# Kernel tuning notes

Measured on AMD Instinct MI355X. Metric: run time of the kernel, lower is better.

Reference implementation:

```python
import jax, jax.numpy as jnp
import numpy as np

N_EMBED = 1024
N_HEADS = 16
HEAD_SIZE = N_EMBED // N_HEADS
BLOCK_SIZE = 256
LN_EPS = 1e-5


def _layernorm(x, g, b):
    mu = jnp.mean(x, axis=-1, keepdims=True)
    var = jnp.var(x, axis=-1, keepdims=True)
    return (x - mu) * jax.lax.rsqrt(var + LN_EPS) * g + b


def setup_inputs() -> dict:
    key = jax.random.key(0)
    ks = jax.random.split(key, 12)
    B, T, C, H, D = 64, 256, N_EMBED, N_HEADS, HEAD_SIZE
    s = lambda fan_in: 1.0 / np.sqrt(fan_in)
    return {
        "x": jax.random.normal(ks[0], (B, T, C), jnp.float32),
        # per-head Q/K/V projections (bias=False in torch), stacked over heads
        "Wq": jax.random.uniform(ks[1], (H, C, D), jnp.float32, -s(C), s(C)),
        "Wk": jax.random.uniform(ks[2], (H, C, D), jnp.float32, -s(C), s(C)),
        "Wv": jax.random.uniform(ks[3], (H, C, D), jnp.float32, -s(C), s(C)),
        "Wproj": jax.random.uniform(ks[4], (C, C), jnp.float32, -s(C), s(C)),
        "bproj": jax.random.uniform(ks[5], (C,), jnp.float32, -s(C), s(C)),
        "W1": jax.random.uniform(ks[6], (C, 4 * C), jnp.float32, -s(C), s(C)),
        "b1": jax.random.uniform(ks[7], (4 * C,), jnp.float32, -s(C), s(C)),
        "W2": jax.random.uniform(ks[8], (4 * C, C), jnp.float32, -s(4 * C), s(4 * C)),
        "b2": jax.random.uniform(ks[9], (C,), jnp.float32, -s(4 * C), s(4 * C)),
        "ln1_g": jnp.ones((C,), jnp.float32),
        "ln1_b": jnp.zeros((C,), jnp.float32),
        "ln2_g": jnp.ones((C,), jnp.float32),
        "ln2_b": jnp.zeros((C,), jnp.float32),
    }


def reference(x, Wq, Wk, Wv, Wproj, bproj, W1, b1, W2, b2, ln1_g, ln1_b, ln2_g, ln2_b):
    B, T, C = x.shape
    # --- self-attention sub-block ---
    h = _layernorm(x, ln1_g, ln1_b)
    q = jnp.einsum("btc,hcd->bhtd", h, Wq)
    k = jnp.einsum("btc,hcd->bhtd", h, Wk)
    v = jnp.einsum("btc,hcd->bhtd", h, Wv)
    # NOTE: original scales by C**-0.5 with C = n_embed (full dim), not head_size
    scores = jnp.einsum("bhtd,bhsd->bhts", q, k) * (C ** -0.5)
    causal = jnp.tril(jnp.ones((T, T), bool))
    scores = jnp.where(causal, scores, -jnp.inf)
    wei = jax.nn.softmax(scores, axis=-1)
    attn = jnp.einsum("bhts,bhsd->bhtd", wei, v)  # [B,H,T,D]
    attn = attn.transpose(0, 2, 1, 3).reshape(B, T, C)  # concat heads
    x = x + attn @ Wproj + bproj
    # --- feed-forward sub-block ---
    h2 = _layernorm(x, ln2_g, ln2_b)
    ffn = jax.nn.relu(h2 @ W1 + b1) @ W2 + b2
    return x + ffn
```

## Files before the change

kernel.cpp:

```cpp
#include <hip/hip_runtime.h>
#include <stdint.h>

using u16 = unsigned short;
using u32 = unsigned int;

typedef __attribute__((ext_vector_type(8))) short s16x8;
typedef __attribute__((ext_vector_type(4))) float f32x4;

__device__ __forceinline__ float bflo(u32 u) { u32 t = u << 16; float f; __builtin_memcpy(&f, &t, 4); return f; }
__device__ __forceinline__ float bfhi(u32 u) { u32 t = u & 0xffff0000u; float f; __builtin_memcpy(&f, &t, 4); return f; }
__device__ __forceinline__ u16 f2bf(float f) {
  u32 u; __builtin_memcpy(&u, &f, 4);
  return (u16)((u + 0x7fffu + ((u >> 16) & 1u)) >> 16);
}

__device__ __forceinline__ void gload_lds16(const void* g, void* l) {
  __builtin_amdgcn_global_load_lds((const __attribute__((address_space(1))) void*)g,
                                   (__attribute__((address_space(3))) void*)l, 16, 0, 0);
}

__global__ __launch_bounds__(256)
void transpose_pack(const float* __restrict__ in, u16* __restrict__ out,
                    int R, int Cc, long in_bs, long out_bs)
{
  __shared__ float tile[32][33];
  in  += (size_t)blockIdx.z * in_bs;
  out += (size_t)blockIdx.z * out_bs;
  const int r0 = blockIdx.x * 32, c0 = blockIdx.y * 32;
  const int tx = threadIdx.x & 31, ty = threadIdx.x >> 5;
#pragma unroll
  for (int i = 0; i < 4; ++i) {
    int r = ty + i * 8;
    tile[r][tx] = in[(size_t)(r0 + r) * Cc + c0 + tx];
  }
  __syncthreads();
#pragma unroll
  for (int i = 0; i < 4; ++i) {
    int c = ty + i * 8;
    out[(size_t)(c0 + c) * R + r0 + tx] = f2bf(tile[tx][c]);
  }
}

__global__ __launch_bounds__(256)
void ln_f32_bf16(const float* __restrict__ x, const float* __restrict__ g,
                 const float* __restrict__ bta, u16* __restrict__ out)
{
  const int row = blockIdx.x, tid = threadIdx.x;
  const float4 v = ((const float4*)(x + (size_t)row * 1024))[tid];
  float s  = v.x + v.y + v.z + v.w;
  float ss = v.x * v.x + v.y * v.y + v.z * v.z + v.w * v.w;
#pragma unroll
  for (int m = 1; m < 64; m <<= 1) {
    s  += __shfl_xor(s, m);
    ss += __shfl_xor(ss, m);
  }
  __shared__ float red[8];
  const int wave = tid >> 6, lane = tid & 63;
  if (lane == 0) { red[wave] = s; red[4 + wave] = ss; }
  __syncthreads();
  s  = red[0] + red[1] + red[2] + red[3];
  ss = red[4] + red[5] + red[6] + red[7];
  const float mu  = s * (1.f / 1024.f);
  const float var = ss * (1.f / 1024.f) - mu * mu;
  const float rs  = rsqrtf(var + 1e-5f);
  const float4 gg = ((const float4*)g)[tid];
  const float4 bb = ((const float4*)bta)[tid];
  u32 w0 = (u32)f2bf((v.x - mu) * rs * gg.x + bb.x) | ((u32)f2bf((v.y - mu) * rs * gg.y + bb.y) << 16);
  u32 w1 = (u32)f2bf((v.z - mu) * rs * gg.z + bb.z) | ((u32)f2bf((v.w - mu) * rs * gg.w + bb.w) << 16);
  u32* outp = (u32*)(out + (size_t)row * 1024 + tid * 4);
  outp[0] = w0; outp[1] = w1;
}

template <int EPI>
__global__ __launch_bounds__(512, 1)
void gemm8p(const u16* __restrict__ A, const u16* __restrict__ B, void* __restrict__ Cv,
            const float* __restrict__ bias, const float* __restrict__ resid,
            int M, int N, int K, int GM)
{
  __shared__ u16 lds[65536];
  const int NT = K >> 6;
  const int tid = threadIdx.x;
  const int lane = tid & 63, wv = tid >> 6;
  const int wr = wv >> 2, wc = wv & 3;
  const int r = lane & 15, kg = lane >> 4;

  const int nwg = gridDim.x;
  const int q = nwg >> 3;
  const int bid = blockIdx.x;
  const int sw = (bid & 7) * q + (bid >> 3);
  const int bn = sw / GM, bm = sw % GM;

  const u16* Ab = A + (size_t)bm * 256 * K;
  const u16* Bb = B + (size_t)bn * 256 * K;

  const int segx = (kg ^ ((r >> 1) & 3)) << 3;
  const int aoff = (wr * 128 + r) * 32 + segx;
  const int boff = 32768 + (wc * 64 + r) * 32 + segx;

  f32x4 acc[8][4];
#pragma unroll
  for (int m = 0; m < 8; ++m)
#pragma unroll
    for (int n = 0; n < 4; ++n) acc[m][n] = f32x4{0.f, 0.f, 0.f, 0.f};

  auto stage = [&](const u16* src, int u, int kh, int base) {
#pragma unroll
    for (int jj = 0; jj < 2; ++jj) {
      int ci = jj * 512 + tid;
      int row = ci >> 2;
      int sseg = (ci & 3) ^ ((ci >> 3) & 3);
      gload_lds16(src + (size_t)row * K + u * 64 + kh * 32 + sseg * 8, &lds[base + ci * 8]);
    }
  };

  stage(Ab, 0, 0, 0);
  stage(Bb, 0, 0, 32768);
  stage(Ab, 0, 1, 8192);
  stage(Bb, 0, 1, 32768 + 8192);
  if (NT > 1) {
    stage(Ab, 1, 0, 16384);
    stage(Bb, 1, 0, 32768 + 16384);
    asm volatile("s_waitcnt vmcnt(4)" ::: "memory");
  } else {
    asm volatile("s_waitcnt vmcnt(0)" ::: "memory");
  }
  __builtin_amdgcn_s_barrier();
  __builtin_amdgcn_sched_barrier(0);

  for (int t = 0; t < NT; ++t) {
    const int buf = t & 1;
    const int ab = buf * 16384;
    const bool s1 = (t + 1) < NT, s2 = (t + 2) < NT;
    s16x8 av[4], bv[4];

#pragma unroll
    for (int m = 0; m < 4; ++m) av[m] = *(const s16x8*)&lds[ab + aoff + m * 512];
#pragma unroll
    for (int n = 0; n < 4; ++n) bv[n] = *(const s16x8*)&lds[ab + boff + n * 512];
    if (s1) stage(Ab, t + 1, 1, (buf ^ 1) * 16384 + 8192);
    __builtin_amdgcn_s_barrier();
    __builtin_amdgcn_sched_barrier(0);
    __builtin_amdgcn_s_setprio(1);
#pragma unroll
    for (int m = 0; m < 4; ++m)
#pragma unroll
      for (int n = 0; n < 4; ++n)
        acc[m][n] = __builtin_amdgcn_mfma_f32_16x16x32_bf16(av[m], bv[n], acc[m][n], 0, 0, 0);
    __builtin_amdgcn_s_setprio(0);
    __builtin_amdgcn_sched_barrier(0);
    __builtin_amdgcn_s_barrier();
    __builtin_amdgcn_sched_barrier(0);

#pragma unroll
    for (int m = 0; m < 4; ++m) av[m] = *(const s16x8*)&lds[ab + aoff + (m + 4) * 512];
    if (s1) stage(Bb, t + 1, 1, 32768 + (buf ^ 1) * 16384 + 8192);
    __builtin_amdgcn_s_barrier();
    __builtin_amdgcn_sched_barrier(0);
    __builtin_amdgcn_s_setprio(1);
#pragma unroll
    for (int m = 0; m < 4; ++m)
#pragma unroll
      for (int n = 0; n < 4; ++n)
        acc[m + 4][n] = __builtin_amdgcn_mfma_f32_16x16x32_bf16(av[m], bv[n], acc[m + 4][n], 0, 0, 0);
    __builtin_amdgcn_s_setprio(0);
    __builtin_amdgcn_sched_barrier(0);
    __builtin_amdgcn_s_barrier();
    __builtin_amdgcn_sched_barrier(0);

#pragma unroll
    for (int m = 0; m < 4; ++m) av[m] = *(const s16x8*)&lds[ab + aoff + 8192 + m * 512];
#pragma unroll
    for (int n = 0; n < 4; ++n) bv[n] = *(const s16x8*)&lds[ab + boff + 8192 + n * 512];
    if (s2) stage(Ab, t + 2, 0, buf * 16384);
    __builtin_amdgcn_s_barrier();
    __builtin_amdgcn_sched_barrier(0);
    __builtin_amdgcn_s_setprio(1);
#pragma unroll
    for (int m = 0; m < 4; ++m)
#pragma unroll
      for (int n = 0; n < 4; ++n)
        acc[m][n] = __builtin_amdgcn_mfma_f32_16x16x32_bf16(av[m], bv[n], acc[m][n], 0, 0, 0);
    __builtin_amdgcn_s_setprio(0);
    __builtin_amdgcn_sched_barrier(0);
    __builtin_amdgcn_s_barrier();
    __builtin_amdgcn_sched_barrier(0);

#pragma unroll
    for (int m = 0; m < 4; ++m) av[m] = *(const s16x8*)&lds[ab + aoff + 8192 + (m + 4) * 512];
    if (s2) stage(Bb, t + 2, 0, 32768 + buf * 16384);
    __builtin_amdgcn_s_barrier();
    __builtin_amdgcn_sched_barrier(0);
    __builtin_amdgcn_s_setprio(1);
#pragma unroll
    for (int m = 0; m < 4; ++m)
#pragma unroll
      for (int n = 0; n < 4; ++n)
        acc[m + 4][n] = __builtin_amdgcn_mfma_f32_16x16x32_bf16(av[m], bv[n], acc[m + 4][n], 0, 0, 0);
    __builtin_amdgcn_s_setprio(0);
    __builtin_amdgcn_sched_barrier(0);
    if (s2) asm volatile("s_waitcnt vmcnt(4)" ::: "memory");
    else    asm volatile("s_waitcnt vmcnt(0)" ::: "memory");
    __builtin_amdgcn_s_barrier();
    __builtin_amdgcn_sched_barrier(0);
  }

#pragma unroll
  for (int m = 0; m < 8; ++m) {
#pragma unroll
    for (int n = 0; n < 4; ++n) {
#pragma unroll
      for (int j = 0; j < 4; ++j) {
        int row = bm * 256 + wr * 128 + m * 16 + kg * 4 + j;
        int col = bn * 256 + wc * 64 + n * 16 + r;
        size_t idx = (size_t)row * N + col;
        float v = acc[m][n][j];
        if constexpr (EPI == 0) {
          ((u16*)Cv)[idx] = f2bf(v);
        } else if constexpr (EPI == 1) {
          ((float*)Cv)[idx] = v + bias[col] + resid[idx];
        } else if constexpr (EPI == 2) {
          ((u16*)Cv)[idx] = f2bf(fmaxf(v + bias[col], 0.f));
        } else {
          ((float*)Cv)[idx] = v + bias[col] + resid[idx];
        }
      }
    }
  }
}

__global__ __launch_bounds__(256)
void attn_mfma(const u16* __restrict__ qkv, u16* __restrict__ outc)
{
  const int bh = blockIdx.x, b = bh >> 4, h = bh & 15;
  const int tid = threadIdx.x;
  const int lane = tid & 63, w = tid >> 6;
  const int r = lane & 15, kg = lane >> 4;

  __shared__ u16 Ks[64 * 64];
  __shared__ u16 Vt[64 * 72];
  __shared__ u16 P[4][64 * 72];

  const u16* qbase = qkv + (size_t)(b * 256) * 3072 + h * 64;

  s16x8 qf[4][2];
#pragma unroll
  for (int m = 0; m < 4; ++m)
#pragma unroll
    for (int ks = 0; ks < 2; ++ks)
      qf[m][ks] = *(const s16x8*)(qbase + (size_t)(w * 64 + m * 16 + r) * 3072 + ks * 32 + kg * 8);

  f32x4 of[4][4];
  float mrun[4][4], lrun[4][4];
#pragma unroll
  for (int m = 0; m < 4; ++m) {
#pragma unroll
    for (int n = 0; n < 4; ++n) of[m][n] = f32x4{0.f, 0.f, 0.f, 0.f};
#pragma unroll
    for (int j = 0; j < 4; ++j) { mrun[m][j] = -1e30f; lrun[m][j] = 0.f; }
  }

  const float cexp = 0.03125f * 1.4426950408889634f;

  for (int kt = 0; kt < 4; ++kt) {
#pragma unroll
    for (int jj = 0; jj < 2; ++jj) {
      int ci = jj * 256 + tid;
      int key = ci >> 3, seg = ci & 7;
      int sseg = seg ^ (key & 7);
      gload_lds16(qkv + (size_t)(b * 256 + kt * 64 + key) * 3072 + 1024 + h * 64 + sseg * 8,
                  &Ks[ci * 8]);
    }
    {
      int row = tid >> 2, q = tid & 3;
      const u16* vg = qkv + (size_t)(b * 256 + kt * 64 + row) * 3072 + 2048 + h * 64 + q * 16;
      union { uint4 u[2]; u16 s[16]; } vv;
      vv.u[0] = *(const uint4*)vg;
      vv.u[1] = *(const uint4*)(vg + 8);
#pragma unroll
      for (int i = 0; i < 16; ++i)
        Vt[(q * 16 + i) * 72 + row] = vv.s[i];
    }
    __syncthreads();

    if (w >= kt) {
      f32x4 s[4][4];
#pragma unroll
      for (int m = 0; m < 4; ++m)
#pragma unroll
        for (int n = 0; n < 4; ++n) s[m][n] = f32x4{0.f, 0.f, 0.f, 0.f};
#pragma unroll
      for (int ks = 0; ks < 2; ++ks) {
        s16x8 kb[4];
#pragma unroll
        for (int n = 0; n < 4; ++n) {
          int row = n * 16 + r;
          int sseg = (ks * 4 + kg) ^ (row & 7);
          kb[n] = *(const s16x8*)&Ks[row * 64 + sseg * 8];
        }
#pragma unroll
        for (int m = 0; m < 4; ++m)
#pragma unroll
          for (int n = 0; n < 4; ++n)
            s[m][n] = __builtin_amdgcn_mfma_f32_16x16x32_bf16(qf[m][ks], kb[n], s[m][n], 0, 0, 0);
      }
      if (kt == w) {
#pragma unroll
        for (int m = 0; m < 4; ++m)
#pragma unroll
          for (int n = 0; n < 4; ++n)
#pragma unroll
            for (int j = 0; j < 4; ++j)
              if (n * 16 + r > m * 16 + kg * 4 + j) s[m][n][j] = -1e30f;
      }
#pragma unroll
      for (int m = 0; m < 4; ++m) {
        float rm[4], rsc[4], ls[4];
#pragma unroll
        for (int j = 0; j < 4; ++j) {
          rm[j] = fmaxf(fmaxf(s[m][0][j], s[m][1][j]), fmaxf(s[m][2][j], s[m][3][j]));
          rm[j] = fmaxf(rm[j], __shfl_xor(rm[j], 1));
          rm[j] = fmaxf(rm[j], __shfl_xor(rm[j], 2));
          rm[j] = fmaxf(rm[j], __shfl_xor(rm[j], 4));
          rm[j] = fmaxf(rm[j], __shfl_xor(rm[j], 8));
          float mnew = fmaxf(mrun[m][j], rm[j]);
          rsc[j] = exp2f((mrun[m][j] - mnew) * cexp);
          mrun[m][j] = mnew;
          ls[j] = 0.f;
        }
#pragma unroll
        for (int n = 0; n < 4; ++n)
#pragma unroll
          for (int j = 0; j < 4; ++j) {
            float p = exp2f((s[m][n][j] - mrun[m][j]) * cexp);
            ls[j] += p;
            P[w][(m * 16 + kg * 4 + j) * 72 + n * 16 + r] = f2bf(p);
          }
#pragma unroll
        for (int j = 0; j < 4; ++j) {
          ls[j] += __shfl_xor(ls[j], 1);
          ls[j] += __shfl_xor(ls[j], 2);
          ls[j] += __shfl_xor(ls[j], 4);
          ls[j] += __shfl_xor(ls[j], 8);
          lrun[m][j] = lrun[m][j] * rsc[j] + ls[j];
        }
#pragma unroll
        for (int n = 0; n < 4; ++n)
#pragma unroll
          for (int j = 0; j < 4; ++j)
            of[m][n][j] *= rsc[j];
      }
#pragma unroll
      for (int kk = 0; kk < 2; ++kk) {
        s16x8 pa[4], vb[4];
#pragma unroll
        for (int m = 0; m < 4; ++m)
          pa[m] = *(const s16x8*)&P[w][(m * 16 + r) * 72 + kk * 32 + kg * 8];
#pragma unroll
        for (int n = 0; n < 4; ++n)
          vb[n] = *(const s16x8*)&Vt[(n * 16 + r) * 72 + kk * 32 + kg * 8];
#pragma unroll
        for (int m = 0; m < 4; ++m)
#pragma unroll
          for (int n = 0; n < 4; ++n)
            of[m][n] = __builtin_amdgcn_mfma_f32_16x16x32_bf16(pa[m], vb[n], of[m][n], 0, 0, 0);
      }
    }
    __syncthreads();
  }

#pragma unroll
  for (int m = 0; m < 4; ++m) {
    float inv[4];
#pragma unroll
    for (int j = 0; j < 4; ++j) inv[j] = 1.f / lrun[m][j];
#pragma unroll
    for (int n = 0; n < 4; ++n)
#pragma unroll
      for (int j = 0; j < 4; ++j) {
        int row = b * 256 + w * 64 + m * 16 + kg * 4 + j;
        outc[(size_t)row * 1024 + h * 64 + n * 16 + r] = f2bf(of[m][n][j] * inv[j]);
      }
  }
}

extern "C" void kernel_launch(void* const* d_in, const int* in_sizes, int n_in,
                              void* d_out, int out_size, void* d_ws, size_t ws_size,
                              hipStream_t stream) {
  (void)in_sizes; (void)n_in; (void)out_size; (void)ws_size;
  const float* x     = (const float*)d_in[0];
  const float* Wq    = (const float*)d_in[1];
  const float* Wk    = (const float*)d_in[2];
  const float* Wv    = (const float*)d_in[3];
  const float* Wproj = (const float*)d_in[4];
  const float* bproj = (const float*)d_in[5];
  const float* W1    = (const float*)d_in[6];
  const float* b1    = (const float*)d_in[7];
  const float* W2    = (const float*)d_in[8];
  const float* b2    = (const float*)d_in[9];
  const float* ln1g  = (const float*)d_in[10];
  const float* ln1b  = (const float*)d_in[11];
  const float* ln2g  = (const float*)d_in[12];
  const float* ln2b  = (const float*)d_in[13];
  float* out = (float*)d_out;

  char* ws = (char*)d_ws;
  u16*   WqkvT  = (u16*)(ws + 0);
  u16*   WprojT = (u16*)(ws + 6291456);
  u16*   W1T    = (u16*)(ws + 8388608);
  u16*   W2T    = (u16*)(ws + 16777216);
  u16*   hb     = (u16*)(ws + 25165824);
  u16*   qkvb   = (u16*)(ws + 58720256);
  float* x2     = (float*)(ws + 159383552);
  u16*   h2     = (u16*)(ws + 226492416);
  u16*   ffn1   = (u16*)(ws + 25165824);
  u16*   attnout = hb;

  const int M = 16384;

  transpose_pack<<<dim3(32, 2, 16), 256, 0, stream>>>(Wq, WqkvT,           1024, 64, 65536, 65536);
  transpose_pack<<<dim3(32, 2, 16), 256, 0, stream>>>(Wk, WqkvT + 1048576, 1024, 64, 65536, 65536);
  transpose_pack<<<dim3(32, 2, 16), 256, 0, stream>>>(Wv, WqkvT + 2097152, 1024, 64, 65536, 65536);
  transpose_pack<<<dim3(32, 32, 1), 256, 0, stream>>>(Wproj, WprojT, 1024, 1024, 0, 0);
  transpose_pack<<<dim3(32, 128, 1), 256, 0, stream>>>(W1, W1T, 1024, 4096, 0, 0);
  transpose_pack<<<dim3(128, 32, 1), 256, 0, stream>>>(W2, W2T, 4096, 1024, 0, 0);

  ln_f32_bf16<<<M, 256, 0, stream>>>(x, ln1g, ln1b, hb);

  gemm8p<0><<<64 * 12, 512, 0, stream>>>(hb, WqkvT, qkvb, nullptr, nullptr, M, 3072, 1024, 64);

  attn_mfma<<<1024, 256, 0, stream>>>(qkvb, attnout);

  gemm8p<1><<<64 * 4, 512, 0, stream>>>(attnout, WprojT, x2, bproj, x, M, 1024, 1024, 64);

  ln_f32_bf16<<<M, 256, 0, stream>>>(x2, ln2g, ln2b, h2);

  gemm8p<2><<<64 * 16, 512, 0, stream>>>(h2, W1T, ffn1, b1, nullptr, M, 4096, 1024, 64);

  gemm8p<3><<<64 * 4, 512, 0, stream>>>(ffn1, W2T, out, b2, x2, M, 1024, 4096, 64);
}
```

Baseline: 643.0 us.

## Merge GEMM main loop from four barrier-separated phases into two

The bf16 MFMA GEMM inner loop went from four sub-phases, each with its own s_barrier pair, to two. Each half-tile phase now loads all 8 A fragments and 4 B fragments from LDS, then issues 32 MFMAs. The A and B global-to-LDS stages for each half are issued together at the start of each phase. This is meant to cut barrier and scheduling overhead and give the compiler larger MFMA blocks to overlap with LDS reads. In exchange it holds more VGPRs for A fragments and drops several sched_barriers, which may change the instruction interleaving or occupancy.

```diff
diff --git a/kernel.cpp b/kernel.cpp
--- a/kernel.cpp
+++ b/kernel.cpp
@@ -131,77 +131,45 @@
     const int buf = t & 1;
     const int ab = buf * 16384;
     const bool s1 = (t + 1) < NT, s2 = (t + 2) < NT;
-    s16x8 av[4], bv[4];
-
-#pragma unroll
-    for (int m = 0; m < 4; ++m) av[m] = *(const s16x8*)&lds[ab + aoff + m * 512];
+    s16x8 av[8], bv[4];
+
+    if (s1) {
+      stage(Ab, t + 1, 1, (buf ^ 1) * 16384 + 8192);
+      stage(Bb, t + 1, 1, 32768 + (buf ^ 1) * 16384 + 8192);
+    }
 #pragma unroll
     for (int n = 0; n < 4; ++n) bv[n] = *(const s16x8*)&lds[ab + boff + n * 512];
-    if (s1) stage(Ab, t + 1, 1, (buf ^ 1) * 16384 + 8192);
-    __builtin_amdgcn_s_barrier();
-    __builtin_amdgcn_sched_barrier(0);
+#pragma unroll
+    for (int m = 0; m < 8; ++m) av[m] = *(const s16x8*)&lds[ab + aoff + m * 512];
     __builtin_amdgcn_s_setprio(1);
 #pragma unroll
-    for (int m = 0; m < 4; ++m)
+    for (int m = 0; m < 8; ++m)
 #pragma unroll
       for (int n = 0; n < 4; ++n)
         acc[m][n] = __builtin_amdgcn_mfma_f32_16x16x32_bf16(av[m], bv[n], acc[m][n], 0, 0, 0);
     __builtin_amdgcn_s_setprio(0);
     __builtin_amdgcn_sched_barrier(0);
     __builtin_amdgcn_s_barrier();
-    __builtin_amdgcn_sched_barrier(0);
-
-#pragma unroll
-    for (int m = 0; m < 4; ++m) av[m] = *(const s16x8*)&lds[ab + aoff + (m + 4) * 512];
-    if (s1) stage(Bb, t + 1, 1, 32768 + (buf ^ 1) * 16384 + 8192);
-    __builtin_amdgcn_s_barrier();
-    __builtin_amdgcn_sched_barrier(0);
+
+    if (s2) {
+      stage(Ab, t + 2, 0, ab);
+      stage(Bb, t + 2, 0, 32768 + ab);
+    }
+#pragma unroll
+    for (int n = 0; n < 4; ++n) bv[n] = *(const s16x8*)&lds[ab + boff + 8192 + n * 512];
+#pragma unroll
+    for (int m = 0; m < 8; ++m) av[m] = *(const s16x8*)&lds[ab + aoff + 8192 + m * 512];
     __builtin_amdgcn_s_setprio(1);
 #pragma unroll
-    for (int m = 0; m < 4; ++m)
-#pragma unroll
-      for (int n = 0; n < 4; ++n)
-        acc[m + 4][n] = __builtin_amdgcn_mfma_f32_16x16x32_bf16(av[m], bv[n], acc[m + 4][n], 0, 0, 0);
-    __builtin_amdgcn_s_setprio(0);
-    __builtin_amdgcn_sched_barrier(0);
-    __builtin_amdgcn_s_barrier();
-    __builtin_amdgcn_sched_barrier(0);
-
-#pragma unroll
-    for (int m = 0; m < 4; ++m) av[m] = *(const s16x8*)&lds[ab + aoff + 8192 + m * 512];
-#pragma unroll
-    for (int n = 0; n < 4; ++n) bv[n] = *(const s16x8*)&lds[ab + boff + 8192 + n * 512];
-    if (s2) stage(Ab, t + 2, 0, buf * 16384);
-    __builtin_amdgcn_s_barrier();
-    __builtin_amdgcn_sched_barrier(0);
-    __builtin_amdgcn_s_setprio(1);
-#pragma unroll
-    for (int m = 0; m < 4; ++m)
+    for (int m = 0; m < 8; ++m)
 #pragma unroll
       for (int n = 0; n < 4; ++n)
         acc[m][n] = __builtin_amdgcn_mfma_f32_16x16x32_bf16(av[m], bv[n], acc[m][n], 0, 0, 0);
-    __builtin_amdgcn_s_setprio(0);
-    __builtin_amdgcn_sched_barrier(0);
-    __builtin_amdgcn_s_barrier();
-    __builtin_amdgcn_sched_barrier(0);
-
-#pragma unroll
-    for (int m = 0; m < 4; ++m) av[m] = *(const s16x8*)&lds[ab + aoff + 8192 + (m + 4) * 512];
-    if (s2) stage(Bb, t + 2, 0, 32768 + buf * 16384);
-    __builtin_amdgcn_s_barrier();
-    __builtin_amdgcn_sched_barrier(0);
-    __builtin_amdgcn_s_setprio(1);
-#pragma unroll
-    for (int m = 0; m < 4; ++m)
-#pragma unroll
-      for (int n = 0; n < 4; ++n)
-        acc[m + 4][n] = __builtin_amdgcn_mfma_f32_16x16x32_bf16(av[m], bv[n], acc[m + 4][n], 0, 0, 0);
     __builtin_amdgcn_s_setprio(0);
     __builtin_amdgcn_sched_barrier(0);
     if (s2) asm volatile("s_waitcnt vmcnt(4)" ::: "memory");
     else    asm volatile("s_waitcnt vmcnt(0)" ::: "memory");
     __builtin_amdgcn_s_barrier();
-    __builtin_amdgcn_sched_barrier(0);
   }
 
 #pragma unroll
```

Measured after the change: 650.4 us. About the same (+1.1%).
